# Performance work log

Hardware: AMD Instinct MI355X
Metric: run time of the kernel (lower is better)

The kernel has to match this reference:

```python
import jax, jax.numpy as jnp
import numpy as np

T, B = 32, 64
H, W = 16, 16
FEAT = 32
CNN_DIM = 512
N_ACT = 5
MAP_OUT = FEAT * H * W  # 8192, flattened map readout


def _conv_relu(x, w, b, stride):
    y = jax.lax.conv_general_dilated(
        x, w, (stride, stride), 'VALID',
        dimension_numbers=('NCHW', 'OIHW', 'NCHW'))
    return jax.nn.relu(y + b[None, :, None, None])


def _mlp(x, w1, b1, w2, b2):
    return jax.nn.relu(x @ w1 + b1) @ w2 + b2


def setup_inputs() -> dict:
    key = jax.random.key(0)
    ks = jax.random.split(key, 32)
    g = lambda k, shape, fan: jax.random.normal(k, shape, jnp.float32) * (1.0 / np.sqrt(fan))
    inp = {}
    inp['image'] = jax.random.uniform(ks[0], (T * B, 84, 84, 3), jnp.float32) * 255.0
    inp['done'] = jnp.zeros((T, B), jnp.float32)
    inp['state0'] = jnp.zeros((B, FEAT, H, W), jnp.float32)
    inp['position'] = jax.random.randint(ks[1], (T * B, 2), 0, H).astype(jnp.int32)
    # NatureCNN params
    inp['w1'] = g(ks[2], (32, 3, 8, 8), 3 * 8 * 8); inp['b1'] = jnp.zeros((32,), jnp.float32)
    inp['w2'] = g(ks[3], (64, 32, 4, 4), 32 * 4 * 4); inp['b2'] = jnp.zeros((64,), jnp.float32)
    inp['w3'] = g(ks[4], (64, 64, 3, 3), 64 * 3 * 3); inp['b3'] = jnp.zeros((64,), jnp.float32)
    inp['wfc'] = g(ks[5], (64 * 7 * 7, CNN_DIM), 64 * 7 * 7); inp['bfc'] = jnp.zeros((CNN_DIM,), jnp.float32)
    # Map write projection
    inp['Ww'] = g(ks[6], (CNN_DIM, FEAT), CNN_DIM); inp['bw'] = jnp.zeros((FEAT,), jnp.float32)
    # pos_net MLP: one-hot(16)+one-hot(16)=32 -> 64
    inp['wp1'] = g(ks[7], (2 * H, 64), 2 * H); inp['bp1'] = jnp.zeros((64,), jnp.float32)
    inp['wp2'] = g(ks[8], (64, 64), 64); inp['bp2'] = jnp.zeros((64,), jnp.float32)
    # policy MLP: (MAP_OUT+64) -> 64 -> N_ACT
    inp['wpo1'] = g(ks[9], (MAP_OUT + 64, 64), MAP_OUT + 64); inp['bpo1'] = jnp.zeros((64,), jnp.float32)
    inp['wpo2'] = g(ks[10], (64, N_ACT), 64) * 0.01; inp['bpo2'] = jnp.zeros((N_ACT,), jnp.float32)
    # value MLP
    inp['wv1'] = g(ks[11], (MAP_OUT + 64, 64), MAP_OUT + 64); inp['bv1'] = jnp.zeros((64,), jnp.float32)
    inp['wv2'] = g(ks[12], (64, 1), 64); inp['bv2'] = jnp.zeros((1,), jnp.float32)
    return inp


def reference(image, done, state0, w1, b1, w2, b2, w3, b3, wfc, bfc, Ww, bw,
              wp1, bp1, wp2, bp2, wpo1, bpo1, wpo2, bpo2, wv1, bv1, wv2, bv2,
              position):
    # preprocess_image: /255 and NHWC -> NCHW
    x = jnp.transpose(image / 255.0, (0, 3, 1, 2))
    x = _conv_relu(x, w1, b1, 4)   # [TB,32,20,20]
    x = _conv_relu(x, w2, b2, 2)   # [TB,64,9,9]
    x = _conv_relu(x, w3, b3, 1)   # [TB,64,7,7]
    h = jax.nn.relu(x.reshape(x.shape[0], -1) @ wfc + bfc)  # [TB,512]

    h_seq = h.reshape(T, B, CNN_DIM)
    idx_seq = position.reshape(T, B, 2)
    benv = jnp.arange(B)

    def step(state, inp):
        h_t, d_t, i_t = inp
        masked = (1.0 - d_t)[:, None, None, None] * state  # reset done envs
        wfeat = h_t @ Ww + bw                              # [B,FEAT]
        state = masked.at[benv, :, i_t[:, 0], i_t[:, 1]].add(wfeat)
        return state, state.reshape(B, -1)                 # per-step map readout

    state, outs = jax.lax.scan(step, state0, (h_seq, done, idx_seq))
    hidden = outs.reshape(T * B, MAP_OUT)

    # position net on one-hot coords
    pos_oh = jnp.concatenate([jax.nn.one_hot(position[:, 0], H, dtype=hidden.dtype),
                              jax.nn.one_hot(position[:, 1], W, dtype=hidden.dtype)], axis=1)
    pos_feat = _mlp(pos_oh, wp1, bp1, wp2, bp2)            # [TB,64]
    hidden = jnp.concatenate([hidden, pos_feat], axis=1)

    logits = _mlp(hidden, wpo1, bpo1, wpo2, bpo2)          # [TB,N_ACT]
    v = _mlp(hidden, wv1, bv1, wv2, bv2)                   # [TB,1]
    return logits, v, state
```

## Files before the change

kernel.cpp:

```cpp
#include <hip/hip_runtime.h>
#include <hip/hip_bf16.h>


#define TT 32
#define BB 64
#define TBR 2048

typedef _Float16 half_t;
typedef __attribute__((ext_vector_type(4))) _Float16 half4;
typedef __attribute__((ext_vector_type(8))) _Float16 half8;
typedef __attribute__((ext_vector_type(4))) float f32x4;

#define OFF_W1T   0u
#define OFF_W2T   6144u
#define OFF_W3T   22528u
#define OFF_WF    40960u
#define OFF_PF    106496u
#define OFF_Y0    237568u
#define OFF_YS    245760u
#define OFF_H     507904u
#define OFF_WFCT  1556480u
#define OFF_C3    2359296u
#define OFF_C2    5570560u
#define OFF_C1    10878976u

__global__ __launch_bounds__(256) void prep_kernel(
    const float* __restrict__ w1, const float* __restrict__ w2,
    const float* __restrict__ w3, half_t* __restrict__ w1p,
    half_t* __restrict__ w2T, half_t* __restrict__ w3T) {
  int g = blockIdx.x * 256 + threadIdx.x;
  if (g < 8192) {
    int kk = g & 31, oc = (g >> 5) & 31, tap = g >> 10;
    half_t v = (half_t)0.f;
    if (kk < 24) {
      int kx = kk / 3, c = kk - 3 * kx;
      v = (half_t)(w1[oc * 192 + c * 64 + tap * 8 + kx] * (1.0f / 255.0f));
    }
    w1p[g] = v;
    return;
  }
  int g2 = g - 8192;
  if (g2 < 32768) {
    int c = g2 & 31, oc = (g2 >> 5) & 63, tap = g2 >> 11;
    w2T[g2] = (half_t)w2[oc * 512 + c * 16 + tap];
    return;
  }
  int g3 = g2 - 32768;
  if (g3 < 36864) {
    int c = g3 & 63, oc = (g3 >> 6) & 63, tap = g3 >> 12;
    w3T[g3] = (half_t)w3[oc * 576 + c * 9 + tap];
  }
}

__global__ __launch_bounds__(256) void prep_wfct(
    const float* __restrict__ wfc, half_t* __restrict__ wfcT) {
  __shared__ float t[32][33];
  int k0 = blockIdx.x * 32, n0 = blockIdx.y * 32;
  int tx = threadIdx.x & 31, ty = threadIdx.x >> 5;
#pragma unroll
  for (int i = 0; i < 4; ++i)
    t[ty + 8 * i][tx] = wfc[(size_t)(k0 + ty + 8 * i) * 512 + n0 + tx];
  __syncthreads();
#pragma unroll
  for (int i = 0; i < 4; ++i)
    wfcT[(size_t)(n0 + ty + 8 * i) * 3136 + k0 + tx] =
        (half_t)t[tx][ty + 8 * i];
}

#define C1_BANDF 5040
#define C1_BANDV 1260
__global__ __launch_bounds__(256) void conv1_mfma(
    const float* __restrict__ img, const half_t* __restrict__ w1p,
    const float* __restrict__ b1, half_t* __restrict__ out, int n0) {
  __shared__ __align__(16) half_t As[2][C1_BANDF];
  int tid = threadIdx.x;
  int li = blockIdx.x;
  int w = tid >> 6, l = tid & 63, lc = l & 15, q = l >> 4;
  const float* ib = img + (size_t)(n0 + li) * 21168;
  half_t* ob = out + (size_t)li * 400 * 32;

  half8 bfrag[8][2];
#pragma unroll
  for (int tap = 0; tap < 8; ++tap)
#pragma unroll
    for (int t = 0; t < 2; ++t)
      bfrag[tap][t] =
          *(const half8*)(w1p + (size_t)(tap * 32 + t * 16 + lc) * 32 + q * 8);
  float b1v[2] = {b1[lc], b1[16 + lc]};

  f32x4 fr[5];
#define C1_LOADB(b)                                                   \
  {                                                                   \
    const float* src = ib + 4032 * (b);                               \
    _Pragma("unroll") for (int i = 0; i < 5; ++i) {                   \
      int g = tid + 256 * i;                                          \
      if (g < C1_BANDV) fr[i] = *(const f32x4*)(src + 4 * g);         \
    }                                                                 \
  }
#define C1_WRITEB(buf)                                                \
  {                                                                   \
    _Pragma("unroll") for (int i = 0; i < 5; ++i) {                   \
      int g = tid + 256 * i;                                          \
      if (g < C1_BANDV) {                                             \
        half4 o;                                                      \
        _Pragma("unroll") for (int j = 0; j < 4; ++j)                 \
            o[j] = (half_t)fr[i][j];                                  \
        *(half4*)&As[buf][4 * g] = o;                                 \
      }                                                               \
    }                                                                 \
  }

  C1_LOADB(0);
  C1_WRITEB(0);
  for (int b = 0; b < 5; ++b) {
    if (b < 4) C1_LOADB(b + 1);
    __syncthreads();
    int buf = b & 1;
    for (int tile = w; tile < 5; tile += 4) {
      int lp = tile * 16 + lc;
      int oyl = lp / 20, ox = lp - oyl * 20;
      f32x4 acc[2];
      acc[0] = (f32x4){0.f, 0.f, 0.f, 0.f};
      acc[1] = (f32x4){0.f, 0.f, 0.f, 0.f};
#pragma unroll
      for (int ky = 0; ky < 8; ++ky) {
        half8 af;
        if (q < 3) {
          const half_t* p = &As[buf][(4 * oyl + ky) * 252 + 12 * ox + q * 8];
          *(half4*)&af = *(const half4*)p;
          *((half4*)&af + 1) = *((const half4*)(p + 4));
        } else {
#pragma unroll
          for (int j = 0; j < 8; ++j) af[j] = (half_t)0.f;
        }
        acc[0] = __builtin_amdgcn_mfma_f32_16x16x32_f16(af, bfrag[ky][0],
                                                        acc[0], 0, 0, 0);
        acc[1] = __builtin_amdgcn_mfma_f32_16x16x32_f16(af, bfrag[ky][1],
                                                        acc[1], 0, 0, 0);
      }
#pragma unroll
      for (int t = 0; t < 2; ++t) {
#pragma unroll
        for (int r = 0; r < 4; ++r) {
          int mr = b * 80 + tile * 16 + q * 4 + r;
          ob[(size_t)mr * 32 + t * 16 + lc] =
              (half_t)fmaxf(acc[t][r] + b1v[t], 0.f);
        }
      }
    }
    if (b < 4) C1_WRITEB((b + 1) & 1);
  }
}

__global__ __launch_bounds__(256) void conv2_mfma(
    const half_t* __restrict__ in, const half_t* __restrict__ w2T,
    const float* __restrict__ b2, half_t* __restrict__ out) {
  __shared__ __align__(16) half_t As[64 * 40];
  __shared__ __align__(16) half_t Bs[64 * 40];
  int tid = threadIdx.x;
  int m0 = blockIdx.x * 64;
  int w = tid >> 6, l = tid & 63, lc = l & 15, q = l >> 4;
  int srow = tid >> 2, sseg = tid & 3;
  int m = m0 + srow;
  int li = m / 81, pos = m - li * 81;
  int oy = pos / 9, ox = pos - (pos / 9) * 9;
  const half_t* aBase = in + (size_t)((li * 20 + 2 * oy) * 20 + 2 * ox) * 32 + sseg * 8;
  const half_t* bBase = w2T + srow * 32 + sseg * 8;
  uint4 aReg = *(const uint4*)aBase;
  uint4 bReg = *(const uint4*)bBase;
  f32x4 acc[4];
#pragma unroll
  for (int t = 0; t < 4; ++t) acc[t] = (f32x4){0.f, 0.f, 0.f, 0.f};
#pragma unroll
  for (int tap = 0; tap < 16; ++tap) {
    __syncthreads();
    *(uint4*)&As[srow * 40 + sseg * 8] = aReg;
    *(uint4*)&Bs[srow * 40 + sseg * 8] = bReg;
    __syncthreads();
    if (tap < 15) {
      int nt = tap + 1, ky = nt >> 2, kx = nt & 3;
      aReg = *(const uint4*)(aBase + (ky * 20 + kx) * 32);
      bReg = *(const uint4*)(bBase + nt * 2048);
    }
    half8 af = *(const half8*)&As[(w * 16 + lc) * 40 + q * 8];
#pragma unroll
    for (int t = 0; t < 4; ++t) {
      half8 bf = *(const half8*)&Bs[(t * 16 + lc) * 40 + q * 8];
      acc[t] = __builtin_amdgcn_mfma_f32_16x16x32_f16(af, bf, acc[t], 0, 0, 0);
    }
  }
#pragma unroll
  for (int t = 0; t < 4; ++t) {
#pragma unroll
    for (int r = 0; r < 4; ++r) {
      int mr = m0 + w * 16 + q * 4 + r;
      int col = t * 16 + lc;
      out[(size_t)mr * 64 + col] = (half_t)fmaxf(acc[t][r] + b2[col], 0.f);
    }
  }
}

__global__ __launch_bounds__(256) void conv3_mfma(
    const half_t* __restrict__ in, const half_t* __restrict__ w3T,
    const float* __restrict__ b3, half_t* __restrict__ out) {
  __shared__ __align__(16) half_t As[64 * 40];
  __shared__ __align__(16) half_t Bs[64 * 40];
  int tid = threadIdx.x;
  int m0 = blockIdx.x * 64;
  int w = tid >> 6, l = tid & 63, lc = l & 15, q = l >> 4;
  int srow = tid >> 2, sseg = tid & 3;
  int m = m0 + srow;
  int li = m / 49, pos = m - li * 49;
  int oy = pos / 7, ox = pos - (pos / 7) * 7;
  const half_t* aBase = in + (size_t)((li * 9 + oy) * 9 + ox) * 64 + sseg * 8;
  const half_t* bBase = w3T + srow * 64 + sseg * 8;
  uint4 aReg = *(const uint4*)aBase;
  uint4 bReg = *(const uint4*)bBase;
  f32x4 acc[4];
#pragma unroll
  for (int t = 0; t < 4; ++t) acc[t] = (f32x4){0.f, 0.f, 0.f, 0.f};
#pragma unroll
  for (int s = 0; s < 18; ++s) {
    __syncthreads();
    *(uint4*)&As[srow * 40 + sseg * 8] = aReg;
    *(uint4*)&Bs[srow * 40 + sseg * 8] = bReg;
    __syncthreads();
    if (s < 17) {
      int ns = s + 1, tap = ns >> 1, ch = ns & 1;
      int ky = tap / 3, kx = tap - ky * 3;
      aReg = *(const uint4*)(aBase + ((ky * 9 + kx) * 64 + ch * 32));
      bReg = *(const uint4*)(bBase + (tap * 4096 + ch * 32));
    }
    half8 af = *(const half8*)&As[(w * 16 + lc) * 40 + q * 8];
#pragma unroll
    for (int t = 0; t < 4; ++t) {
      half8 bf = *(const half8*)&Bs[(t * 16 + lc) * 40 + q * 8];
      acc[t] = __builtin_amdgcn_mfma_f32_16x16x32_f16(af, bf, acc[t], 0, 0, 0);
    }
  }
#pragma unroll
  for (int t = 0; t < 4; ++t) {
#pragma unroll
    for (int r = 0; r < 4; ++r) {
      int mr = m0 + w * 16 + q * 4 + r;
      int li2 = mr / 49, pos2 = mr - li2 * 49;
      int col = t * 16 + lc;
      out[(size_t)li2 * 3136 + col * 49 + pos2] =
          (half_t)fmaxf(acc[t][r] + b3[col], 0.f);
    }
  }
}

__global__ __launch_bounds__(256) void fc_mfma(
    const half_t* __restrict__ A, const half_t* __restrict__ Bt,
    const float* __restrict__ bias, float* __restrict__ C) {
  __shared__ __align__(16) half_t As[64 * 40];
  __shared__ __align__(16) half_t Bs[64 * 40];
  int tid = threadIdx.x;
  int m0 = blockIdx.y * 64, n0 = blockIdx.x * 64;
  int w = tid >> 6;
  int l = tid & 63;
  int lc = l & 15, q = l >> 4;
  int srow = tid >> 2, sseg = tid & 3;

  const half_t* aPtr = A + (size_t)(m0 + srow) * 3136 + sseg * 8;
  const half_t* bPtr = Bt + (size_t)(n0 + srow) * 3136 + sseg * 8;
  uint4 aReg = *(const uint4*)aPtr;
  uint4 bReg = *(const uint4*)bPtr;

  f32x4 acc[4];
#pragma unroll
  for (int t = 0; t < 4; ++t) acc[t] = (f32x4){0.f, 0.f, 0.f, 0.f};

  for (int k0 = 0; k0 < 3136; k0 += 32) {
    __syncthreads();
    *(uint4*)&As[srow * 40 + sseg * 8] = aReg;
    *(uint4*)&Bs[srow * 40 + sseg * 8] = bReg;
    __syncthreads();
    if (k0 + 32 < 3136) {
      aReg = *(const uint4*)(aPtr + k0 + 32);
      bReg = *(const uint4*)(bPtr + k0 + 32);
    }
    half8 af = *(const half8*)&As[(w * 16 + lc) * 40 + q * 8];
#pragma unroll
    for (int t = 0; t < 4; ++t) {
      half8 bf = *(const half8*)&Bs[(t * 16 + lc) * 40 + q * 8];
      acc[t] = __builtin_amdgcn_mfma_f32_16x16x32_f16(af, bf, acc[t], 0, 0, 0);
    }
  }
#pragma unroll
  for (int t = 0; t < 4; ++t) {
#pragma unroll
    for (int r = 0; r < 4; ++r) {
      int row = m0 + w * 16 + q * 4 + r;
      int col = n0 + t * 16 + lc;
      C[(size_t)row * 512 + col] = fmaxf(acc[t][r] + bias[col], 0.f);
    }
  }
}

__global__ __launch_bounds__(256) void wfeat_kernel(
    const float* __restrict__ h, const float* __restrict__ Ww,
    const float* __restrict__ bw, float* __restrict__ wf) {
  int g = blockIdx.x * 256 + threadIdx.x;
  int row = g >> 5, oc = g & 31;
  float acc = bw[oc];
  const float* hr = h + (size_t)row * 512;
#pragma unroll 8
  for (int k = 0; k < 512; ++k) acc += hr[k] * Ww[k * 32 + oc];
  wf[g] = acc;
}

__global__ __launch_bounds__(256) void posfeat_kernel(
    const int* __restrict__ pos, const float* __restrict__ wp1,
    const float* __restrict__ bp1, const float* __restrict__ wp2,
    const float* __restrict__ bp2, float* __restrict__ pf) {
  int row = (blockIdx.x * 256 + threadIdx.x) >> 6;
  int l = threadIdx.x & 63;
  int p0 = pos[row * 2], p1 = pos[row * 2 + 1];
  float t1 = fmaxf(wp1[p0 * 64 + l] + wp1[(16 + p1) * 64 + l] + bp1[l], 0.f);
  float acc = bp2[l];
#pragma unroll
  for (int k = 0; k < 64; ++k) acc += __shfl(t1, k) * wp2[k * 64 + l];
  pf[row * 64 + l] = acc;
}

__global__ __launch_bounds__(256) void y0_kernel(
    const float* __restrict__ s0, const float* __restrict__ wpo1,
    const float* __restrict__ wv1, float* __restrict__ y0) {
  __shared__ float red[128];
  int b = blockIdx.x >> 5, kc = blockIdx.x & 31;
  int n = threadIdx.x & 127, kh = threadIdx.x >> 7;
  const float* W = (n < 64) ? (wpo1 + n) : (wv1 + (n - 64));
  int k0 = kc * 256 + kh * 128;
  const float* s = s0 + (size_t)b * 8192 + k0;
  float acc = 0.f;
#pragma unroll 8
  for (int j = 0; j < 128; ++j) acc += s[j] * W[(size_t)(k0 + j) * 64];
  if (kh) red[n] = acc;
  __syncthreads();
  if (!kh) atomicAdd(y0 + b * 128 + n, acc + red[n]);
}

__global__ __launch_bounds__(128) void ystate_kernel(
    const float* __restrict__ y0, const float* __restrict__ done,
    const int* __restrict__ pos, const float* __restrict__ wf,
    const float* __restrict__ wpo1, const float* __restrict__ wv1,
    float* __restrict__ ys) {
  int b = blockIdx.x;
  int n = threadIdx.x;
  const float* W = (n < 64) ? (wpo1 + n) : (wv1 + (n - 64));
  float y = y0[b * 128 + n];
  for (int t = 0; t < TT; ++t) {
    int row = t * BB + b;
    float mask = 1.f - done[row];
    int off = pos[row * 2] * 16 + pos[row * 2 + 1];
    y *= mask;
    const float* wfr = wf + row * 32;
#pragma unroll
    for (int c = 0; c < 32; ++c) y += wfr[c] * W[(size_t)(c * 256 + off) * 64];
    ys[(size_t)row * 128 + n] = y;
  }
}

__global__ __launch_bounds__(256) void state_kernel(
    const float* __restrict__ s0, const float* __restrict__ done,
    const int* __restrict__ pos, const float* __restrict__ wf,
    float* __restrict__ out_state) {
  int b = blockIdx.x, tid = threadIdx.x;
  float s[32];
#pragma unroll
  for (int c = 0; c < 32; ++c) s[c] = s0[(size_t)b * 8192 + c * 256 + tid];
  for (int t = 0; t < TT; ++t) {
    int row = t * BB + b;
    float mask = 1.f - done[row];
    int off = pos[row * 2] * 16 + pos[row * 2 + 1];
#pragma unroll
    for (int c = 0; c < 32; ++c) s[c] *= mask;
    if (tid == off) {
#pragma unroll
      for (int c = 0; c < 32; ++c) s[c] += wf[row * 32 + c];
    }
  }
#pragma unroll
  for (int c = 0; c < 32; ++c) out_state[(size_t)b * 8192 + c * 256 + tid] = s[c];
}

__global__ __launch_bounds__(256) void head_kernel(
    const float* __restrict__ ys, const float* __restrict__ pf,
    const float* __restrict__ wpo1, const float* __restrict__ wv1,
    const float* __restrict__ bpo1, const float* __restrict__ bv1,
    const float* __restrict__ wpo2, const float* __restrict__ bpo2,
    const float* __restrict__ wv2, const float* __restrict__ bv2,
    float* __restrict__ logits, float* __restrict__ vout) {
  int row = (blockIdx.x * 256 + threadIdx.x) >> 6;
  int l = threadIdx.x & 63;
  float pfv = pf[row * 64 + l];
  float accp = bpo1[l] + ys[(size_t)row * 128 + l];
  float accv = bv1[l] + ys[(size_t)row * 128 + 64 + l];
#pragma unroll
  for (int k = 0; k < 64; ++k) {
    float pk = __shfl(pfv, k);
    accp += pk * wpo1[(size_t)(8192 + k) * 64 + l];
    accv += pk * wv1[(size_t)(8192 + k) * 64 + l];
  }
  float rp = fmaxf(accp, 0.f), rv = fmaxf(accv, 0.f);
#pragma unroll
  for (int a = 0; a < 5; ++a) {
    float pa = rp * wpo2[l * 5 + a];
#pragma unroll
    for (int m = 32; m >= 1; m >>= 1) pa += __shfl_xor(pa, m);
    if (l == 0) logits[row * 5 + a] = pa + bpo2[a];
  }
  float pv = rv * wv2[l];
#pragma unroll
  for (int m = 32; m >= 1; m >>= 1) pv += __shfl_xor(pv, m);
  if (l == 0) vout[row] = pv + bv2[0];
}

extern "C" void kernel_launch(void* const* d_in, const int* in_sizes, int n_in,
                              void* d_out, int out_size, void* d_ws, size_t ws_size,
                              hipStream_t stream) {
  const float* image = (const float*)d_in[0];
  const float* done = (const float*)d_in[1];
  const float* state0 = (const float*)d_in[2];
  const int* position = (const int*)d_in[3];
  const float* w1 = (const float*)d_in[4];
  const float* b1 = (const float*)d_in[5];
  const float* w2 = (const float*)d_in[6];
  const float* b2 = (const float*)d_in[7];
  const float* w3 = (const float*)d_in[8];
  const float* b3 = (const float*)d_in[9];
  const float* wfc = (const float*)d_in[10];
  const float* bfc = (const float*)d_in[11];
  const float* Ww = (const float*)d_in[12];
  const float* bw = (const float*)d_in[13];
  const float* wp1 = (const float*)d_in[14];
  const float* bp1 = (const float*)d_in[15];
  const float* wp2 = (const float*)d_in[16];
  const float* bp2 = (const float*)d_in[17];
  const float* wpo1 = (const float*)d_in[18];
  const float* bpo1 = (const float*)d_in[19];
  const float* wpo2 = (const float*)d_in[20];
  const float* bpo2 = (const float*)d_in[21];
  const float* wv1 = (const float*)d_in[22];
  const float* bv1 = (const float*)d_in[23];
  const float* wv2 = (const float*)d_in[24];
  const float* bv2 = (const float*)d_in[25];

  float* ws = (float*)d_ws;
  half_t* w1p = (half_t*)(ws + OFF_W1T);
  half_t* w2T = (half_t*)(ws + OFF_W2T);
  half_t* w3T = (half_t*)(ws + OFF_W3T);
  float* wf = ws + OFF_WF;
  float* pfb = ws + OFF_PF;
  float* y0 = ws + OFF_Y0;
  float* ysb = ws + OFF_YS;
  float* h = ws + OFF_H;
  half_t* wfcT = (half_t*)(ws + OFF_WFCT);
  half_t* c3b = (half_t*)(ws + OFF_C3);
  half_t* c2b = (half_t*)(ws + OFF_C2);
  half_t* c1b = (half_t*)(ws + OFF_C1);

  float* out = (float*)d_out;
  float* out_logits = out;
  float* out_v = out + 10240;
  float* out_state = out + 12288;

  int CS;
  if (ws_size >= (size_t)23986176 * 4) CS = 2048;
  else if (ws_size >= (size_t)17432576 * 4) CS = 1024;
  else CS = 512;
  int nc = TBR / CS;

  hipMemsetAsync(y0, 0, 8192 * sizeof(float), stream);
  prep_kernel<<<304, 256, 0, stream>>>(w1, w2, w3, w1p, w2T, w3T);
  prep_wfct<<<dim3(98, 16), 256, 0, stream>>>(wfc, wfcT);

  for (int c = 0; c < nc; ++c) {
    int n0 = c * CS;
    conv1_mfma<<<CS, 256, 0, stream>>>(image, w1p, b1, c1b, n0);
    conv2_mfma<<<CS * 81 / 64, 256, 0, stream>>>(
        c1b, w2T, b2, c2b + (size_t)n0 * 5184);
  }
  conv3_mfma<<<TBR * 49 / 64, 256, 0, stream>>>(c2b, w3T, b3, c3b);
  fc_mfma<<<dim3(8, 32), 256, 0, stream>>>(c3b, wfcT, bfc, h);
  wfeat_kernel<<<256, 256, 0, stream>>>(h, Ww, bw, wf);
  posfeat_kernel<<<512, 256, 0, stream>>>(position, wp1, bp1, wp2, bp2, pfb);
  y0_kernel<<<2048, 256, 0, stream>>>(state0, wpo1, wv1, y0);
  ystate_kernel<<<64, 128, 0, stream>>>(y0, done, position, wf, wpo1, wv1, ysb);
  state_kernel<<<64, 256, 0, stream>>>(state0, done, position, wf, out_state);
  head_kernel<<<512, 256, 0, stream>>>(ysb, pfb, wpo1, wv1, bpo1, bv1,
                                       wpo2, bpo2, wv2, bv2, out_logits, out_v);
}
```

Baseline: 524.8 us.

## Restructure conv2/conv3 as per-image blocks with LDS-resident inputs and register weights

```diff
diff --git a/kernel.cpp b/kernel.cpp
--- a/kernel.cpp
+++ b/kernel.cpp
@@ -154,48 +154,73 @@
 
 __global__ __launch_bounds__(256) void conv2_mfma(
     const half_t* __restrict__ in, const half_t* __restrict__ w2T,
-    const float* __restrict__ b2, half_t* __restrict__ out) {
-  __shared__ __align__(16) half_t As[64 * 40];
-  __shared__ __align__(16) half_t Bs[64 * 40];
+    const float* __restrict__ b2, half_t* __restrict__ out, int n0) {
+  __shared__ __align__(16) half_t As[12800];
   int tid = threadIdx.x;
-  int m0 = blockIdx.x * 64;
+  int li = blockIdx.x;
   int w = tid >> 6, l = tid & 63, lc = l & 15, q = l >> 4;
-  int srow = tid >> 2, sseg = tid & 3;
-  int m = m0 + srow;
-  int li = m / 81, pos = m - li * 81;
-  int oy = pos / 9, ox = pos - (pos / 9) * 9;
-  const half_t* aBase = in + (size_t)((li * 20 + 2 * oy) * 20 + 2 * ox) * 32 + sseg * 8;
-  const half_t* bBase = w2T + srow * 32 + sseg * 8;
-  uint4 aReg = *(const uint4*)aBase;
-  uint4 bReg = *(const uint4*)bBase;
-  f32x4 acc[4];
-#pragma unroll
-  for (int t = 0; t < 4; ++t) acc[t] = (f32x4){0.f, 0.f, 0.f, 0.f};
-#pragma unroll
-  for (int tap = 0; tap < 16; ++tap) {
-    __syncthreads();
-    *(uint4*)&As[srow * 40 + sseg * 8] = aReg;
-    *(uint4*)&Bs[srow * 40 + sseg * 8] = bReg;
-    __syncthreads();
-    if (tap < 15) {
-      int nt = tap + 1, ky = nt >> 2, kx = nt & 3;
-      aReg = *(const uint4*)(aBase + (ky * 20 + kx) * 32);
-      bReg = *(const uint4*)(bBase + nt * 2048);
-    }
-    half8 af = *(const half8*)&As[(w * 16 + lc) * 40 + q * 8];
-#pragma unroll
-    for (int t = 0; t < 4; ++t) {
-      half8 bf = *(const half8*)&Bs[(t * 16 + lc) * 40 + q * 8];
-      acc[t] = __builtin_amdgcn_mfma_f32_16x16x32_f16(af, bf, acc[t], 0, 0, 0);
-    }
-  }
-#pragma unroll
-  for (int t = 0; t < 4; ++t) {
-#pragma unroll
-    for (int r = 0; r < 4; ++r) {
-      int mr = m0 + w * 16 + q * 4 + r;
-      int col = t * 16 + lc;
-      out[(size_t)mr * 64 + col] = (half_t)fmaxf(acc[t][r] + b2[col], 0.f);
+  const half_t* inb = in + (size_t)li * 12800;
+
+#pragma unroll
+  for (int i = 0; i < 7; ++i) {
+    int ci = tid + 256 * i;
+    if (ci < 1600) {
+      uint4 v = *(const uint4*)(inb + ci * 8);
+      int ip = ci >> 2, sp = ip >> 1;
+      int u = ((ip & 1) << 6) | ((ci & 3) << 4);
+      int byte = sp * 128 + (u ^ ((sp & 7) << 4));
+      *(uint4*)((char*)As + byte) = v;
+    }
+  }
+
+  half8 bfrag[16][2];
+#pragma unroll
+  for (int tap = 0; tap < 16; ++tap)
+#pragma unroll
+    for (int j = 0; j < 2; ++j) {
+      int nt = (w & 1) * 2 + j;
+      bfrag[tap][j] =
+          *(const half8*)(w2T + (size_t)(tap * 64 + nt * 16 + lc) * 32 + q * 8);
+    }
+  float b2v[2];
+#pragma unroll
+  for (int j = 0; j < 2; ++j) b2v[j] = b2[(w & 1) * 32 + j * 16 + lc];
+
+  __syncthreads();
+
+  half_t* ob = out + (size_t)(n0 + li) * 5184;
+#pragma unroll
+  for (int ti = 0; ti < 3; ++ti) {
+    int tile = (w >> 1) + 2 * ti;
+    int row16 = tile * 16 + lc;
+    int orow = row16 < 81 ? row16 : 80;
+    int oy = orow / 9, ox = orow - oy * 9;
+    f32x4 acc[2];
+    acc[0] = (f32x4){0.f, 0.f, 0.f, 0.f};
+    acc[1] = (f32x4){0.f, 0.f, 0.f, 0.f};
+#pragma unroll
+    for (int tap = 0; tap < 16; ++tap) {
+      int ky = tap >> 2, kx = tap & 3;
+      int ip = (2 * oy + ky) * 20 + 2 * ox + kx;
+      int sp = ip >> 1;
+      int u = ((ip & 1) << 6) | (q << 4);
+      int byte = sp * 128 + (u ^ ((sp & 7) << 4));
+      half8 af = *(const half8*)((const char*)As + byte);
+      acc[0] = __builtin_amdgcn_mfma_f32_16x16x32_f16(af, bfrag[tap][0],
+                                                      acc[0], 0, 0, 0);
+      acc[1] = __builtin_amdgcn_mfma_f32_16x16x32_f16(af, bfrag[tap][1],
+                                                      acc[1], 0, 0, 0);
+    }
+#pragma unroll
+    for (int j = 0; j < 2; ++j) {
+#pragma unroll
+      for (int r = 0; r < 4; ++r) {
+        int mr = tile * 16 + q * 4 + r;
+        if (mr < 81) {
+          int col = (w & 1) * 32 + j * 16 + lc;
+          ob[(size_t)mr * 64 + col] = (half_t)fmaxf(acc[j][r] + b2v[j], 0.f);
+        }
+      }
     }
   }
 }
@@ -203,50 +228,60 @@
 __global__ __launch_bounds__(256) void conv3_mfma(
     const half_t* __restrict__ in, const half_t* __restrict__ w3T,
     const float* __restrict__ b3, half_t* __restrict__ out) {
-  __shared__ __align__(16) half_t As[64 * 40];
-  __shared__ __align__(16) half_t Bs[64 * 40];
+  __shared__ __align__(16) half_t As[5184];
   int tid = threadIdx.x;
-  int m0 = blockIdx.x * 64;
+  int li = blockIdx.x;
   int w = tid >> 6, l = tid & 63, lc = l & 15, q = l >> 4;
-  int srow = tid >> 2, sseg = tid & 3;
-  int m = m0 + srow;
-  int li = m / 49, pos = m - li * 49;
-  int oy = pos / 7, ox = pos - (pos / 7) * 7;
-  const half_t* aBase = in + (size_t)((li * 9 + oy) * 9 + ox) * 64 + sseg * 8;
-  const half_t* bBase = w3T + srow * 64 + sseg * 8;
-  uint4 aReg = *(const uint4*)aBase;
-  uint4 bReg = *(const uint4*)bBase;
-  f32x4 acc[4];
-#pragma unroll
-  for (int t = 0; t < 4; ++t) acc[t] = (f32x4){0.f, 0.f, 0.f, 0.f};
-#pragma unroll
-  for (int s = 0; s < 18; ++s) {
-    __syncthreads();
-    *(uint4*)&As[srow * 40 + sseg * 8] = aReg;
-    *(uint4*)&Bs[srow * 40 + sseg * 8] = bReg;
-    __syncthreads();
-    if (s < 17) {
-      int ns = s + 1, tap = ns >> 1, ch = ns & 1;
+  const half_t* inb = in + (size_t)li * 5184;
+
+#pragma unroll
+  for (int i = 0; i < 3; ++i) {
+    int ci = tid + 256 * i;
+    if (ci < 648) {
+      uint4 v = *(const uint4*)(inb + ci * 8);
+      int ir = ci >> 3, cc = ci & 7;
+      int byte = ir * 128 + (((cc << 4)) ^ ((ir & 7) << 4));
+      *(uint4*)((char*)As + byte) = v;
+    }
+  }
+
+  half8 bfrag[9][2];
+#pragma unroll
+  for (int tap = 0; tap < 9; ++tap)
+#pragma unroll
+    for (int ch = 0; ch < 2; ++ch)
+      bfrag[tap][ch] = *(const half8*)(
+          w3T + (size_t)(tap * 64 + w * 16 + lc) * 64 + ch * 32 + q * 8);
+  float b3v = b3[w * 16 + lc];
+
+  __syncthreads();
+
+  half_t* ob = out + (size_t)li * 3136;
+#pragma unroll
+  for (int tile = 0; tile < 4; ++tile) {
+    int row16 = tile * 16 + lc;
+    int orow = row16 < 49 ? row16 : 48;
+    int oy = orow / 7, ox = orow - oy * 7;
+    f32x4 acc = (f32x4){0.f, 0.f, 0.f, 0.f};
+#pragma unroll
+    for (int tap = 0; tap < 9; ++tap) {
       int ky = tap / 3, kx = tap - ky * 3;
-      aReg = *(const uint4*)(aBase + ((ky * 9 + kx) * 64 + ch * 32));
-      bReg = *(const uint4*)(bBase + (tap * 4096 + ch * 32));
-    }
-    half8 af = *(const half8*)&As[(w * 16 + lc) * 40 + q * 8];
-#pragma unroll
-    for (int t = 0; t < 4; ++t) {
-      half8 bf = *(const half8*)&Bs[(t * 16 + lc) * 40 + q * 8];
-      acc[t] = __builtin_amdgcn_mfma_f32_16x16x32_f16(af, bf, acc[t], 0, 0, 0);
-    }
-  }
-#pragma unroll
-  for (int t = 0; t < 4; ++t) {
+      int ir = (oy + ky) * 9 + ox + kx;
+#pragma unroll
+      for (int ch = 0; ch < 2; ++ch) {
+        int byte = ir * 128 + (((ch << 6) | (q << 4)) ^ ((ir & 7) << 4));
+        half8 af = *(const half8*)((const char*)As + byte);
+        acc = __builtin_amdgcn_mfma_f32_16x16x32_f16(af, bfrag[tap][ch],
+                                                     acc, 0, 0, 0);
+      }
+    }
 #pragma unroll
     for (int r = 0; r < 4; ++r) {
-      int mr = m0 + w * 16 + q * 4 + r;
-      int li2 = mr / 49, pos2 = mr - li2 * 49;
-      int col = t * 16 + lc;
-      out[(size_t)li2 * 3136 + col * 49 + pos2] =
-          (half_t)fmaxf(acc[t][r] + b3[col], 0.f);
+      int pos = tile * 16 + q * 4 + r;
+      if (pos < 49) {
+        int col = w * 16 + lc;
+        ob[(size_t)col * 49 + pos] = (half_t)fmaxf(acc[r] + b3v, 0.f);
+      }
     }
   }
 }
@@ -480,10 +515,9 @@
   for (int c = 0; c < nc; ++c) {
     int n0 = c * CS;
     conv1_mfma<<<CS, 256, 0, stream>>>(image, w1p, b1, c1b, n0);
-    conv2_mfma<<<CS * 81 / 64, 256, 0, stream>>>(
-        c1b, w2T, b2, c2b + (size_t)n0 * 5184);
-  }
-  conv3_mfma<<<TBR * 49 / 64, 256, 0, stream>>>(c2b, w3T, b3, c3b);
+    conv2_mfma<<<CS, 256, 0, stream>>>(c1b, w2T, b2, c2b, n0);
+  }
+  conv3_mfma<<<TBR, 256, 0, stream>>>(c2b, w3T, b3, c3b);
   fc_mfma<<<dim3(8, 32), 256, 0, stream>>>(c3b, wfcT, bfc, h);
   wfeat_kernel<<<256, 256, 0, stream>>>(h, Ww, bw, wf);
   posfeat_kernel<<<512, 256, 0, stream>>>(position, wp1, bp1, wp2, bp2, pfb);
```

Result: no change. 520.0 us (-0.9%).
